# Optimization experiments

Hardware: AMD Instinct MI355X
Metric: run time of the kernel (lower is better)

Reference implementation:

```python
import jax, jax.numpy as jnp
import numpy as np

NC = 20          # num_classes
LAM_COORD = 5.0
LAM_OBJ = 1.0
LAM_NOOBJ = 0.5
LAM_CLS = 1.0


def build_target(gt_boxes, gt_classes, num_box, B, H, W):
    """Vectorized version of the per-object Python loop in Loss.build_target.
    Returns target of shape [B*H*W, NC+5] with layout [one_hot_cls(20), obj, xo, yo, w, h]."""
    M = gt_classes.shape[1]
    valid = jnp.arange(M)[None, :] < num_box[:, None]            # [B, M]
    x = gt_boxes[..., 0] * H                                      # cell units (scale_factor = 1/H)
    y = gt_boxes[..., 1] * H
    gx = jnp.floor(x).astype(jnp.int32)
    gy = jnp.floor(y).astype(jnp.int32)
    # invalid objects scatter into a dummy row H*W which is dropped afterwards
    flat = jnp.where(valid, gy * W + gx, H * W)                   # [B, M]
    vals = jnp.stack([jnp.ones_like(x), x - gx, y - gy,
                      gt_boxes[..., 2] * H, gt_boxes[..., 3] * H], axis=-1)  # [B, M, 5]
    tgt = jnp.zeros((B, H * W + 1, NC + 5), dtype=gt_boxes.dtype)
    bi = jnp.broadcast_to(jnp.arange(B)[:, None], (B, M))
    ch = jnp.arange(NC, NC + 5)
    tgt = tgt.at[bi[:, :, None], flat[:, :, None], ch[None, None, :]].set(vals)
    tgt = tgt.at[bi, flat, gt_classes.astype(jnp.int32)].set(1.0)
    return tgt[:, :H * W].reshape(B * H * W, NC + 5)


def box_iou(a, b):
    """IoU of center-format boxes. a: [N, A, 4], b: [N, 1, 4] -> [N, A]."""
    ax1, ay1 = a[..., 0] - a[..., 2] * 0.5, a[..., 1] - a[..., 3] * 0.5
    ax2, ay2 = a[..., 0] + a[..., 2] * 0.5, a[..., 1] + a[..., 3] * 0.5
    bx1, by1 = b[..., 0] - b[..., 2] * 0.5, b[..., 1] - b[..., 3] * 0.5
    bx2, by2 = b[..., 0] + b[..., 2] * 0.5, b[..., 1] + b[..., 3] * 0.5
    iw = jnp.clip(jnp.minimum(ax2, bx2) - jnp.maximum(ax1, bx1), 0.0)
    ih = jnp.clip(jnp.minimum(ay2, by2) - jnp.maximum(ay1, by1), 0.0)
    inter = iw * ih
    union = a[..., 2] * a[..., 3] + b[..., 2] * b[..., 3] - inter
    return inter / jnp.maximum(union, 1e-10)


def setup_inputs() -> dict:
    key = jax.random.key(0)
    k1, k2, k3, k4 = jax.random.split(key, 4)
    B, H, W, A, M = 256, 32, 32, 5, 50
    anchor = jnp.array([[1.3221, 1.73145], [3.19275, 4.00944], [5.05587, 8.09892],
                        [9.47112, 4.84053], [11.2364, 10.0071]], dtype=jnp.float32)
    out = jax.random.normal(k1, (B, A * (5 + NC), H, W), dtype=jnp.float32)
    gt_boxes = jax.random.uniform(k2, (B, M, 4), dtype=jnp.float32)
    gt_classes = jax.random.randint(k3, (B, M), 0, NC)
    num_box = jax.random.randint(k4, (B,), 0, M)
    return {"out": out, "gt_boxes": gt_boxes, "anchor": anchor,
            "gt_classes": gt_classes, "num_box": num_box}


def reference(out, gt_boxes, anchor, gt_classes, num_box):
    B, _, H, W = out.shape
    A = anchor.shape[0]
    N = B * H * W
    o = jnp.transpose(out, (0, 2, 3, 1)).reshape(N, A, 5 + NC)

    gy, gx = jnp.meshgrid(jnp.arange(H), jnp.arange(W), indexing="ij")
    grid = jnp.stack([gx, gy], axis=-1).reshape(H * W, 2).astype(o.dtype)  # [H*W, 2] (x, y)
    grid = jnp.tile(grid, (B, 1))                                          # [N, 2]

    dxy = jax.nn.sigmoid(o[..., NC + 1:NC + 3])                 # [N, A, 2]
    dwh = jnp.exp(o[..., NC + 3:NC + 5]) * anchor[None]         # [N, A, 2]
    pred_box = jnp.concatenate([grid[:, None] + dxy, dwh], -1)  # [N, A, 4]
    pred_conf = jax.nn.sigmoid(o[..., NC])                      # [N, A]
    pred_cls = o[..., :NC]                                      # [N, A, NC]

    tgt = build_target(gt_boxes, gt_classes, num_box, B, H, W)  # [N, NC+5]
    obj = tgt[:, NC]                                            # [N]
    t_box = jnp.concatenate([grid + tgt[:, NC + 1:NC + 3], tgt[:, NC + 3:NC + 5]], -1)  # [N, 4]

    iou = box_iou(pred_box, t_box[:, None])                     # [N, A]
    best = jnp.argmax(iou, axis=-1)                             # [N]

    pb = jnp.take_along_axis(pred_box, best[:, None, None], 1)[:, 0]   # [N, 4]
    pred_vec = jnp.concatenate([pb[:, :2], jnp.sqrt(pb[:, 2:])], -1)
    t_wh_safe = jnp.where(obj[:, None] > 0, t_box[:, 2:], 1.0)         # guard sqrt(0) grad
    targ_vec = jnp.concatenate([t_box[:, :2], jnp.sqrt(t_wh_safe)], -1)
    box_loss = LAM_COORD / B * jnp.sum(obj[:, None] * (pred_vec - targ_vec) ** 2)

    conf_best = jnp.take_along_axis(pred_conf, best[:, None], 1)[:, 0]
    conf_loss = LAM_OBJ / B * jnp.sum(obj * (conf_best - obj) ** 2)

    mask = obj[:, None] * jax.nn.one_hot(best, A, dtype=o.dtype)        # [N, A]
    noobj_loss = LAM_NOOBJ / B * jnp.sum((1.0 - mask) * pred_conf ** 2)

    logits_best = jnp.take_along_axis(pred_cls, best[:, None, None], 1)[:, 0]  # [N, NC]
    cls_t = jnp.argmax(tgt[:, :NC], axis=-1)
    ce = -jnp.take_along_axis(jax.nn.log_softmax(logits_best, -1), cls_t[:, None], 1)[:, 0]
    cls_loss = LAM_CLS / B * jnp.sum(obj * ce)

    return (box_loss, conf_loss, noobj_loss, cls_loss)
```

## Files before the change

kernel.cpp:

```cpp
#include <hip/hip_runtime.h>

#define NCC 20
#define HH  32
#define WW  32
#define AA  5
#define MM  50
#define HWC (HH*WW)
#define NBLK 1024

__global__ __launch_bounds__(256) void yolo_loss(
    const float* __restrict__ out,
    const float* __restrict__ gt_boxes,
    const float* __restrict__ anchor,
    const int*   __restrict__ gt_classes,
    const int*   __restrict__ num_box,
    float4*      __restrict__ partials)
{
    __shared__ int   s_cell[MM];
    __shared__ float s_xo[MM], s_yo[MM], s_tw[MM], s_th[MM];
    __shared__ int   s_cls[MM];
    __shared__ float s_anc[2*AA];
    __shared__ int   s_nb;
    __shared__ float s_red[4][4];

    const int tid = threadIdx.x;
    const int b   = blockIdx.x >> 2;
    const int rem = ((blockIdx.x & 3) << 8) | tid;

    if (tid == 0) s_nb = num_box[b];
    if (tid < 2*AA) s_anc[tid] = anchor[tid];
    if (tid < MM) {
        float4 g = ((const float4*)gt_boxes)[b*MM + tid];
        float x = g.x * (float)HH;
        float y = g.y * (float)HH;
        int gx = (int)floorf(x);
        int gy = (int)floorf(y);
        s_cell[tid] = gy*WW + gx;
        s_xo[tid] = x - (float)gx;
        s_yo[tid] = y - (float)gy;
        s_tw[tid] = g.z * (float)HH;
        s_th[tid] = g.w * (float)HH;
        s_cls[tid] = gt_classes[b*MM + tid];
    }
    __syncthreads();

    int nb = s_nb; if (nb > MM) nb = MM;

    int clsmask = 0;
    float xo = 0.f, yo = 0.f, tw = 0.f, th = 0.f;
    for (int m = 0; m < nb; ++m) {
        if (s_cell[m] == rem) {
            xo = s_xo[m]; yo = s_yo[m]; tw = s_tw[m]; th = s_th[m];
            clsmask |= 1 << s_cls[m];
        }
    }

    const float* cellp = out + ((size_t)b * (AA*(5+NCC))) * HWC + rem;

    float pc[AA];
    float noobj_l = 0.f;
    #pragma unroll
    for (int a = 0; a < AA; ++a) {
        float cl = cellp[(a*25 + NCC) * HWC];
        float s  = 1.f / (1.f + expf(-cl));
        pc[a] = s;
        noobj_l += s * s;
    }

    float box_l = 0.f, conf_l = 0.f, cls_l = 0.f;

    if (clsmask != 0) {
        const float fgx = (float)(rem & 31);
        const float fgy = (float)(rem >> 5);
        const float tbx = fgx + xo;
        const float tby = fgy + yo;

        float best_iou = -1.f;
        int   best = 0;
        float bpx = 0.f, bpy = 0.f, bpw = 0.f, bph = 0.f;
        #pragma unroll
        for (int a = 0; a < AA; ++a) {
            float t21 = cellp[(a*25 + NCC+1) * HWC];
            float t22 = cellp[(a*25 + NCC+2) * HWC];
            float t23 = cellp[(a*25 + NCC+3) * HWC];
            float t24 = cellp[(a*25 + NCC+4) * HWC];
            float px = fgx + 1.f / (1.f + expf(-t21));
            float py = fgy + 1.f / (1.f + expf(-t22));
            float pw = expf(t23) * s_anc[2*a];
            float ph = expf(t24) * s_anc[2*a+1];
            float iw = fmaxf(fminf(px + pw*0.5f, tbx + tw*0.5f)
                           - fmaxf(px - pw*0.5f, tbx - tw*0.5f), 0.f);
            float ih = fmaxf(fminf(py + ph*0.5f, tby + th*0.5f)
                           - fmaxf(py - ph*0.5f, tby - th*0.5f), 0.f);
            float inter = iw * ih;
            float uni   = pw*ph + tw*th - inter;
            float iou   = inter / fmaxf(uni, 1e-10f);
            if (iou > best_iou) {
                best_iou = iou; best = a;
                bpx = px; bpy = py; bpw = pw; bph = ph;
            }
        }

        float dx = bpx - tbx;
        float dy = bpy - tby;
        float dw = sqrtf(bpw) - sqrtf(tw);
        float dh = sqrtf(bph) - sqrtf(th);
        box_l = dx*dx + dy*dy + dw*dw + dh*dh;

        float cd = pc[best] - 1.f;
        conf_l = cd * cd;

        noobj_l -= pc[best] * pc[best];

        int cls_t = __ffs(clsmask) - 1;
        float mx = -1e30f, ssum = 0.f, lt = 0.f;
        #pragma unroll
        for (int i = 0; i < NCC; ++i) {
            float l = cellp[(best*25 + i) * HWC];
            if (i == cls_t) lt = l;
            float nm = fmaxf(mx, l);
            ssum = ssum * expf(mx - nm) + expf(l - nm);
            mx = nm;
        }
        cls_l = mx + logf(ssum) - lt;
    }

    float v[4] = { box_l  * (5.0f/256.0f),
                   conf_l * (1.0f/256.0f),
                   noobj_l* (0.5f/256.0f),
                   cls_l  * (1.0f/256.0f) };
    const int lane = tid & 63;
    const int wid  = tid >> 6;
    #pragma unroll
    for (int k = 0; k < 4; ++k) {
        float x = v[k];
        #pragma unroll
        for (int off = 32; off > 0; off >>= 1)
            x += __shfl_down(x, off, 64);
        if (lane == 0) s_red[wid][k] = x;
    }
    __syncthreads();
    if (tid == 0) {
        float4 p;
        p.x = s_red[0][0] + s_red[1][0] + s_red[2][0] + s_red[3][0];
        p.y = s_red[0][1] + s_red[1][1] + s_red[2][1] + s_red[3][1];
        p.z = s_red[0][2] + s_red[1][2] + s_red[2][2] + s_red[3][2];
        p.w = s_red[0][3] + s_red[1][3] + s_red[2][3] + s_red[3][3];
        partials[blockIdx.x] = p;
    }
}

__global__ __launch_bounds__(256) void reduce_partials(
    const float4* __restrict__ partials, float* __restrict__ loss)
{
    __shared__ float s_red[4][4];
    const int tid = threadIdx.x;

    float4 a = partials[tid];
    float4 b = partials[tid + 256];
    float4 c = partials[tid + 512];
    float4 d = partials[tid + 768];
    float v[4] = { a.x + b.x + c.x + d.x,
                   a.y + b.y + c.y + d.y,
                   a.z + b.z + c.z + d.z,
                   a.w + b.w + c.w + d.w };

    const int lane = tid & 63;
    const int wid  = tid >> 6;
    #pragma unroll
    for (int k = 0; k < 4; ++k) {
        float x = v[k];
        #pragma unroll
        for (int off = 32; off > 0; off >>= 1)
            x += __shfl_down(x, off, 64);
        if (lane == 0) s_red[wid][k] = x;
    }
    __syncthreads();
    if (tid < 4)
        loss[tid] = s_red[0][tid] + s_red[1][tid] + s_red[2][tid] + s_red[3][tid];
}

extern "C" void kernel_launch(void* const* d_in, const int* in_sizes, int n_in,
                              void* d_out, int out_size, void* d_ws, size_t ws_size,
                              hipStream_t stream) {
    const float* out_t      = (const float*)d_in[0];
    const float* gt_boxes   = (const float*)d_in[1];
    const float* anchor     = (const float*)d_in[2];
    const int*   gt_classes = (const int*)d_in[3];
    const int*   num_box    = (const int*)d_in[4];
    float* loss = (float*)d_out;
    float4* partials = (float4*)d_ws;

    yolo_loss<<<dim3(NBLK), dim3(256), 0, stream>>>(
        out_t, gt_boxes, anchor, gt_classes, num_box, partials);
    reduce_partials<<<dim3(1), dim3(256), 0, stream>>>(partials, loss);
}
```

Before: 180.9 us.

## Scatter targets into shared per-cell table, one block per image

Each block now covers a whole image (1024 threads) instead of a quarter. The per-cell linear scan over up to 50 boxes is replaced by a scatter of box targets into shared-memory per-cell arrays, with last-writer-wins semantics and an atomicOr class mask. This removes the per-thread O(M) loop and the redundant per-quarter preprocessing. It also switches to fast __expf/__logf intrinsics, at a small cost in accuracy, and shrinks the partials reduction to 256 entries. The larger blocks may lower occupancy flexibility.

```diff
diff --git a/kernel.cpp b/kernel.cpp
--- a/kernel.cpp
+++ b/kernel.cpp
@@ -1,14 +1,12 @@
 #include <hip/hip_runtime.h>
 
 #define NCC 20
-#define HH  32
-#define WW  32
 #define AA  5
 #define MM  50
-#define HWC (HH*WW)
-#define NBLK 1024
-
-__global__ __launch_bounds__(256) void yolo_loss(
+#define HWC 1024
+#define NB  256
+
+__global__ __launch_bounds__(1024) void yolo_loss(
     const float* __restrict__ out,
     const float* __restrict__ gt_boxes,
     const float* __restrict__ anchor,
@@ -16,62 +14,73 @@
     const int*   __restrict__ num_box,
     float4*      __restrict__ partials)
 {
+    __shared__ float s_txo[HWC], s_tyo[HWC], s_ttw[HWC], s_tth[HWC];
+    __shared__ int   s_tm[HWC];
     __shared__ int   s_cell[MM];
-    __shared__ float s_xo[MM], s_yo[MM], s_tw[MM], s_th[MM];
-    __shared__ int   s_cls[MM];
     __shared__ float s_anc[2*AA];
     __shared__ int   s_nb;
-    __shared__ float s_red[4][4];
+    __shared__ float s_red[16][4];
 
     const int tid = threadIdx.x;
-    const int b   = blockIdx.x >> 2;
-    const int rem = ((blockIdx.x & 3) << 8) | tid;
-
+    const int b   = blockIdx.x;
+
+    s_tm[tid] = 0;
     if (tid == 0) s_nb = num_box[b];
     if (tid < 2*AA) s_anc[tid] = anchor[tid];
+
+    float oxo = 0.f, oyo = 0.f, otw = 0.f, oth = 0.f;
+    int mycell = 0, mycls = 0;
     if (tid < MM) {
         float4 g = ((const float4*)gt_boxes)[b*MM + tid];
-        float x = g.x * (float)HH;
-        float y = g.y * (float)HH;
+        float x = g.x * 32.f;
+        float y = g.y * 32.f;
         int gx = (int)floorf(x);
         int gy = (int)floorf(y);
-        s_cell[tid] = gy*WW + gx;
-        s_xo[tid] = x - (float)gx;
-        s_yo[tid] = y - (float)gy;
-        s_tw[tid] = g.z * (float)HH;
-        s_th[tid] = g.w * (float)HH;
-        s_cls[tid] = gt_classes[b*MM + tid];
+        mycell = gy*32 + gx;
+        s_cell[tid] = mycell;
+        oxo = x - (float)gx;
+        oyo = y - (float)gy;
+        otw = g.z * 32.f;
+        oth = g.w * 32.f;
+        mycls = gt_classes[b*MM + tid];
     }
     __syncthreads();
 
     int nb = s_nb; if (nb > MM) nb = MM;
-
-    int clsmask = 0;
-    float xo = 0.f, yo = 0.f, tw = 0.f, th = 0.f;
-    for (int m = 0; m < nb; ++m) {
-        if (s_cell[m] == rem) {
-            xo = s_xo[m]; yo = s_yo[m]; tw = s_tw[m]; th = s_th[m];
-            clsmask |= 1 << s_cls[m];
-        }
-    }
-
-    const float* cellp = out + ((size_t)b * (AA*(5+NCC))) * HWC + rem;
+    if (tid < nb) {
+        bool winner = true;
+        for (int m = tid + 1; m < nb; ++m)
+            winner = winner && (s_cell[m] != mycell);
+        if (winner) {
+            s_txo[mycell] = oxo;
+            s_tyo[mycell] = oyo;
+            s_ttw[mycell] = otw;
+            s_tth[mycell] = oth;
+        }
+        atomicOr(&s_tm[mycell], 1 << mycls);
+    }
+    __syncthreads();
+
+    const float* cellp = out + (size_t)b * (AA*25) * HWC + tid;
 
     float pc[AA];
     float noobj_l = 0.f;
     #pragma unroll
     for (int a = 0; a < AA; ++a) {
         float cl = cellp[(a*25 + NCC) * HWC];
-        float s  = 1.f / (1.f + expf(-cl));
+        float s  = 1.f / (1.f + __expf(-cl));
         pc[a] = s;
         noobj_l += s * s;
     }
 
     float box_l = 0.f, conf_l = 0.f, cls_l = 0.f;
+    int clsmask = s_tm[tid];
 
     if (clsmask != 0) {
-        const float fgx = (float)(rem & 31);
-        const float fgy = (float)(rem >> 5);
+        float xo = s_txo[tid], yo = s_tyo[tid];
+        float tw = s_ttw[tid], th = s_tth[tid];
+        const float fgx = (float)(tid & 31);
+        const float fgy = (float)(tid >> 5);
         const float tbx = fgx + xo;
         const float tby = fgy + yo;
 
@@ -84,10 +93,10 @@
             float t22 = cellp[(a*25 + NCC+2) * HWC];
             float t23 = cellp[(a*25 + NCC+3) * HWC];
             float t24 = cellp[(a*25 + NCC+4) * HWC];
-            float px = fgx + 1.f / (1.f + expf(-t21));
-            float py = fgy + 1.f / (1.f + expf(-t22));
-            float pw = expf(t23) * s_anc[2*a];
-            float ph = expf(t24) * s_anc[2*a+1];
+            float px = fgx + 1.f / (1.f + __expf(-t21));
+            float py = fgy + 1.f / (1.f + __expf(-t22));
+            float pw = __expf(t23) * s_anc[2*a];
+            float ph = __expf(t24) * s_anc[2*a+1];
             float iw = fmaxf(fminf(px + pw*0.5f, tbx + tw*0.5f)
                            - fmaxf(px - pw*0.5f, tbx - tw*0.5f), 0.f);
             float ih = fmaxf(fminf(py + ph*0.5f, tby + th*0.5f)
@@ -109,7 +118,6 @@
 
         float cd = pc[best] - 1.f;
         conf_l = cd * cd;
-
         noobj_l -= pc[best] * pc[best];
 
         int cls_t = __ffs(clsmask) - 1;
@@ -119,10 +127,10 @@
             float l = cellp[(best*25 + i) * HWC];
             if (i == cls_t) lt = l;
             float nm = fmaxf(mx, l);
-            ssum = ssum * expf(mx - nm) + expf(l - nm);
+            ssum = ssum * __expf(mx - nm) + __expf(l - nm);
             mx = nm;
         }
-        cls_l = mx + logf(ssum) - lt;
+        cls_l = mx + __logf(ssum) - lt;
     }
 
     float v[4] = { box_l  * (5.0f/256.0f),
@@ -142,11 +150,14 @@
     __syncthreads();
     if (tid == 0) {
         float4 p;
-        p.x = s_red[0][0] + s_red[1][0] + s_red[2][0] + s_red[3][0];
-        p.y = s_red[0][1] + s_red[1][1] + s_red[2][1] + s_red[3][1];
-        p.z = s_red[0][2] + s_red[1][2] + s_red[2][2] + s_red[3][2];
-        p.w = s_red[0][3] + s_red[1][3] + s_red[2][3] + s_red[3][3];
-        partials[blockIdx.x] = p;
+        float s0=0.f, s1=0.f, s2=0.f, s3=0.f;
+        #pragma unroll
+        for (int w = 0; w < 16; ++w) {
+            s0 += s_red[w][0]; s1 += s_red[w][1];
+            s2 += s_red[w][2]; s3 += s_red[w][3];
+        }
+        p.x = s0; p.y = s1; p.z = s2; p.w = s3;
+        partials[b] = p;
     }
 }
 
@@ -156,14 +167,8 @@
     __shared__ float s_red[4][4];
     const int tid = threadIdx.x;
 
-    float4 a = partials[tid];
-    float4 b = partials[tid + 256];
-    float4 c = partials[tid + 512];
-    float4 d = partials[tid + 768];
-    float v[4] = { a.x + b.x + c.x + d.x,
-                   a.y + b.y + c.y + d.y,
-                   a.z + b.z + c.z + d.z,
-                   a.w + b.w + c.w + d.w };
+    float4 p = partials[tid];
+    float v[4] = { p.x, p.y, p.z, p.w };
 
     const int lane = tid & 63;
     const int wid  = tid >> 6;
@@ -191,7 +196,7 @@
     float* loss = (float*)d_out;
     float4* partials = (float4*)d_ws;
 
-    yolo_loss<<<dim3(NBLK), dim3(256), 0, stream>>>(
+    yolo_loss<<<dim3(NB), dim3(1024), 0, stream>>>(
         out_t, gt_boxes, anchor, gt_classes, num_box, partials);
     reduce_partials<<<dim3(1), dim3(256), 0, stream>>>(partials, loss);
 }
```

Result: no change. 181.7 us (+0.5%).
